# Performance work log

Hardware: AMD Instinct MI355X
Metric: run time of the kernel (lower is better)

Reference implementation:

```python
import jax, jax.numpy as jnp
import numpy as np

N_NODES = 20000
N_EDGES = 160000
N_GRAPHS = 64
EMB_DIM = 16
N_BASIS = 16
MAX_RADIUS = 5.0
MUL_IN = 8   # output_size: multiplicity of scalar atom features
MUL_OUT = 4  # multiplicity per output irrep (4x0e + 4x1o + 4x2e -> dim 36)
W_NUMEL = 3 * MUL_IN * MUL_IN * MUL_OUT  # 768 per-edge tensor-product weights


def setup_inputs() -> dict:
    key = jax.random.key(0)
    ks = jax.random.split(key, 16)
    pos = jax.random.normal(ks[0], (N_NODES, 3), jnp.float32) * 3.0
    A = jax.random.randint(ks[1], (N_NODES,), 0, 10)
    batch = jnp.sort(jax.random.randint(ks[2], (N_NODES,), 0, N_GRAPHS))
    edge_src = jax.random.randint(ks[3], (N_EDGES,), 0, N_NODES)
    edge_dst = jax.random.randint(ks[4], (N_EDGES,), 0, N_NODES)
    edge_shifts = jnp.zeros((N_EDGES, 3), jnp.float32)
    cell = jnp.broadcast_to(jnp.eye(3, dtype=jnp.float32) * 10.0, (N_GRAPHS, 3, 3))
    emb_table = jax.random.normal(ks[5], (10, EMB_DIM), jnp.float32)
    fit_w1 = jax.random.normal(ks[6], (EMB_DIM, 64), jnp.float32) * (2.0 / EMB_DIM) ** 0.5
    fit_b1 = jnp.zeros((64,), jnp.float32)
    fit_w2 = jax.random.normal(ks[7], (64, 32), jnp.float32) * (2.0 / 64.0) ** 0.5
    fit_b2 = jnp.zeros((32,), jnp.float32)
    fit_w3 = jax.random.normal(ks[8], (32, MUL_IN), jnp.float32) * (2.0 / 32.0) ** 0.5
    fit_b3 = jnp.zeros((MUL_IN,), jnp.float32)
    fc_w1 = jax.random.normal(ks[9], (N_BASIS, 64), jnp.float32)
    fc_w2 = jax.random.normal(ks[10], (64, 64), jnp.float32)
    fc_w3 = jax.random.normal(ks[11], (64, 64), jnp.float32)
    fc_w4 = jax.random.normal(ks[12], (64, W_NUMEL), jnp.float32)
    return dict(pos=pos, A=A, batch=batch, edge_src=edge_src, edge_dst=edge_dst,
                edge_shifts=edge_shifts, cell=cell, emb_table=emb_table,
                fit_w1=fit_w1, fit_b1=fit_b1, fit_w2=fit_w2, fit_b2=fit_b2,
                fit_w3=fit_w3, fit_b3=fit_b3,
                fc_w1=fc_w1, fc_w2=fc_w2, fc_w3=fc_w3, fc_w4=fc_w4)


def _forward(pos, edge_shifts, cell, emb_table, fit_w1, fit_b1, fit_w2, fit_b2,
             fit_w3, fit_b3, fc_w1, fc_w2, fc_w3, fc_w4, A, batch, edge_src, edge_dst):
    E = edge_src.shape[0]
    # edge vectors with periodic shifts
    shift = jnp.einsum('ni,nij->nj', edge_shifts, cell[batch[edge_src]])
    ev = pos[edge_dst] - pos[edge_src] + shift                     # [E,3]
    r = jnp.sqrt(jnp.sum(ev * ev, axis=1))                         # [E]
    v = ev / jnp.maximum(r, 1e-9)[:, None]
    x, y, z = v[:, 0], v[:, 1], v[:, 2]
    # spherical harmonics lmax=2, normalize=True, 'component' normalization (e3nn order)
    sh0 = jnp.ones_like(x)                                         # [E]
    sh1 = jnp.sqrt(3.0) * jnp.stack([y, z, x], axis=-1)            # [E,3]
    s15 = jnp.sqrt(15.0); s5 = jnp.sqrt(5.0)
    sh2 = jnp.stack([s15 * x * y, s15 * y * z, (s5 / 2.0) * (3.0 * z * z - 1.0),
                     s15 * x * z, (s15 / 2.0) * (x * x - y * y)], axis=-1)  # [E,5]
    # node scalar features: embedding + fitnet MLP (SiLU)
    h = jax.nn.silu(emb_table[A] @ fit_w1 + fit_b1)
    h = jax.nn.silu(h @ fit_w2 + fit_b2)
    Ai = h @ fit_w3 + fit_b3                                       # [N, MUL_IN]
    # soft_one_hot_linspace(gaussian, cutoff=True) * sqrt(n_basis)
    centers = jnp.linspace(0.0, MAX_RADIUS, N_BASIS + 2)[1:-1]
    step = centers[1] - centers[0]
    rb = jnp.exp(-(((r[:, None] - centers) / step) ** 2)) / 1.12 * jnp.sqrt(jnp.float32(N_BASIS))
    # radial net -> per-edge tensor-product weights (e3nn FullyConnectedNet style, no bias)
    g = jax.nn.silu(rb @ fc_w1 / jnp.sqrt(jnp.float32(N_BASIS)))
    g = jax.nn.silu(g @ fc_w2 / 8.0)
    g = jax.nn.silu(g @ fc_w3 / 8.0)
    w = (g @ fc_w4 / 8.0).reshape(E, 3, MUL_IN, MUL_IN, MUL_OUT)   # [E,3 paths,u,v,w]
    # FullTensorProduct(Ai_src, sh) then FullyConnectedTensorProduct(., Ai_dst) with
    # per-edge weights; scalar x irrep paths factorize: out_l[e,w,m] = S_l[e,w]*sh_l[e,m]
    P = Ai[edge_src][:, :, None] * Ai[edge_dst][:, None, :]        # [E,u,v]
    S = jnp.einsum('euv,eluvw->elw', P, w) / jnp.float32(MUL_IN)   # path norm 1/sqrt(u*v)
    out0 = S[:, 0, :] * sh0[:, None]                               # [E,4]
    out1 = (S[:, 1, :, None] * sh1[:, None, :]).reshape(E, MUL_OUT * 3)
    out2 = (S[:, 2, :, None] * sh2[:, None, :]).reshape(E, MUL_OUT * 5)
    ef = jnp.concatenate([out0, out1, out2], axis=-1)              # [E,36]
    # scatter-mean to destination nodes
    cnt = jnp.clip(jax.ops.segment_sum(jnp.ones((E,), ef.dtype), edge_dst,
                                       num_segments=N_NODES), 1.0)
    return jax.ops.segment_sum(ef, edge_dst, num_segments=N_NODES) / cnt[:, None]


def reference(pos, A, batch, edge_src, edge_dst, edge_shifts, cell, emb_table,
              fit_w1, fit_b1, fit_w2, fit_b2, fit_w3, fit_b3,
              fc_w1, fc_w2, fc_w3, fc_w4):
    return _forward(pos, edge_shifts, cell, emb_table, fit_w1, fit_b1, fit_w2,
                    fit_b2, fit_w3, fit_b3, fc_w1, fc_w2, fc_w3, fc_w4,
                    A, batch, edge_src, edge_dst)
```

## Files before the change

kernel.cpp:

```cpp
#include <hip/hip_runtime.h>
#include <math.h>

#define N_NODES 20000
#define N_EDGES 160000

#define NBINS   512
#define BINS1   513
#define RMAX    7.5f

static const size_t OFF_EF  = 0;
static const size_t OFF_T   = OFF_EF  + (size_t)N_EDGES * 16 * 4;
static const size_t OFF_G   = OFF_T   + (size_t)100 * 64 * 12 * 4;
static const size_t OFF_SV  = OFF_G   + (size_t)64 * BINS1 * 4;
static const size_t OFF_NOFF= OFF_SV  + (size_t)100 * BINS1 * 12 * 4;
static const size_t OFF_NCNT= OFF_NOFF+ (size_t)(N_NODES + 1) * 4;
static const size_t OFF_NCUR= OFF_NCNT+ (size_t)N_NODES * 4;

#define P1_T_BLOCKS  25
#define P1_G_BLOCKS  9
#define P1_H_BLOCKS  625
#define P1_GRID (P1_T_BLOCKS + P1_G_BLOCKS + P1_H_BLOCKS)
#define P2_CHUNKS 9
#define P2_GRID (1 + 100 * P2_CHUNKS)

__device__ __forceinline__ float silu_f(float x) {
    return x / (1.0f + __expf(-x));
}

__global__ __launch_bounds__(256) void prep1_kernel(
        const float* __restrict__ emb,
        const float* __restrict__ fw1, const float* __restrict__ fb1,
        const float* __restrict__ fw2, const float* __restrict__ fb2,
        const float* __restrict__ fw3, const float* __restrict__ fb3,
        const float* __restrict__ fc_w1, const float* __restrict__ fc_w2,
        const float* __restrict__ fc_w3, const float* __restrict__ fc_w4,
        const int* __restrict__ edst,
        float* __restrict__ T, float* __restrict__ g_tT,
        int* __restrict__ cnt_i) {
    __shared__ float smem[4096];
    int b = blockIdx.x;
    int tid = threadIdx.x;

    if (b < P1_T_BLOCKS) {
        float* h1s = smem;
        float* h2s = smem + 640;
        float* ai  = smem + 960;
        for (int idx = tid; idx < 640; idx += 256) {
            int t = idx >> 6, j = idx & 63;
            float acc = fb1[j];
            #pragma unroll
            for (int i = 0; i < 16; i++) acc += emb[t * 16 + i] * fw1[i * 64 + j];
            h1s[idx] = silu_f(acc);
        }
        __syncthreads();
        for (int idx = tid; idx < 320; idx += 256) {
            int t = idx >> 5, j = idx & 31;
            float acc = fb2[j];
            #pragma unroll
            for (int i = 0; i < 64; i++) acc += h1s[t * 64 + i] * fw2[i * 32 + j];
            h2s[idx] = silu_f(acc);
        }
        __syncthreads();
        if (tid < 80) {
            int t = tid >> 3, j = tid & 7;
            float acc = fb3[j];
            #pragma unroll
            for (int i = 0; i < 32; i++) acc += h2s[t * 32 + i] * fw3[i * 8 + j];
            ai[tid] = acc;
        }
        __syncthreads();

        int idx = b * 256 + tid;
        int pair = idx >> 6;
        int k = idx & 63;
        int ts = pair / 10, td = pair - ts * 10;
        float a[8], bb[8];
        #pragma unroll
        for (int i = 0; i < 8; i++) a[i] = ai[ts * 8 + i];
        #pragma unroll
        for (int i = 0; i < 8; i++) bb[i] = ai[td * 8 + i];
        float sv[12];
        #pragma unroll
        for (int i = 0; i < 12; i++) sv[i] = 0.0f;
        const float* wk = fc_w4 + k * 768;
        #pragma unroll 2
        for (int u = 0; u < 8; u++) {
            #pragma unroll
            for (int v = 0; v < 8; v++) {
                float ab = a[u] * bb[v];
                const float* wp = wk + u * 32 + v * 4;
                float4 w0 = *(const float4*)(wp);
                float4 w1 = *(const float4*)(wp + 256);
                float4 w2 = *(const float4*)(wp + 512);
                sv[0] += ab * w0.x; sv[1] += ab * w0.y; sv[2]  += ab * w0.z; sv[3]  += ab * w0.w;
                sv[4] += ab * w1.x; sv[5] += ab * w1.y; sv[6]  += ab * w1.z; sv[7]  += ab * w1.w;
                sv[8] += ab * w2.x; sv[9] += ab * w2.y; sv[10] += ab * w2.z; sv[11] += ab * w2.w;
            }
        }
        float* tp = T + pair * 768 + k * 12;
        #pragma unroll
        for (int j = 0; j < 12; j++) tp[j] = sv[j];
    } else if (b < P1_T_BLOCKS + P1_G_BLOCKS) {
        int lane = tid & 63;
        int wq = __builtin_amdgcn_readfirstlane(tid >> 6);
        int bin = (b - P1_T_BLOCKS) * 64 + lane;
        bool valid = (bin <= NBINS);
        float r = (float)bin * (RMAX / (float)NBINS);

        float rb[16];
        const float step = 5.0f / 17.0f;
        const float istep = 17.0f / 5.0f;
        const float rsc = 4.0f / 1.12f;
        #pragma unroll
        for (int i = 0; i < 16; i++) {
            float dd = (r - (float)(i + 1) * step) * istep;
            rb[i] = __expf(-dd * dd) * rsc;
        }

        #pragma unroll
        for (int jj = 0; jj < 16; jj++) {
            int j = wq * 16 + jj;
            float a0 = 0, a1 = 0, a2 = 0, a3 = 0;
            #pragma unroll
            for (int i = 0; i < 16; i += 4) {
                a0 += rb[i]     * fc_w1[(i)     * 64 + j];
                a1 += rb[i + 1] * fc_w1[(i + 1) * 64 + j];
                a2 += rb[i + 2] * fc_w1[(i + 2) * 64 + j];
                a3 += rb[i + 3] * fc_w1[(i + 3) * 64 + j];
            }
            smem[j * 64 + lane] = silu_f(((a0 + a1) + (a2 + a3)) * 0.25f);
        }
        __syncthreads();

        float acc[16];
        #pragma unroll
        for (int jj = 0; jj < 16; jj++) acc[jj] = 0.0f;
        #pragma unroll
        for (int c = 0; c < 4; c++) {
            float hc[16];
            #pragma unroll
            for (int i = 0; i < 16; i++) hc[i] = smem[(c * 16 + i) * 64 + lane];
            #pragma unroll
            for (int jj = 0; jj < 16; jj++) {
                int j = wq * 16 + jj;
                #pragma unroll
                for (int i = 0; i < 16; i++) acc[jj] += hc[i] * fc_w2[(c * 16 + i) * 64 + j];
            }
        }
        __syncthreads();
        #pragma unroll
        for (int jj = 0; jj < 16; jj++) smem[(wq * 16 + jj) * 64 + lane] = silu_f(acc[jj] * 0.125f);
        __syncthreads();

        #pragma unroll
        for (int jj = 0; jj < 16; jj++) acc[jj] = 0.0f;
        #pragma unroll
        for (int c = 0; c < 4; c++) {
            float hc[16];
            #pragma unroll
            for (int i = 0; i < 16; i++) hc[i] = smem[(c * 16 + i) * 64 + lane];
            #pragma unroll
            for (int jj = 0; jj < 16; jj++) {
                int j = wq * 16 + jj;
                #pragma unroll
                for (int i = 0; i < 16; i++) acc[jj] += hc[i] * fc_w3[(c * 16 + i) * 64 + j];
            }
        }
        if (valid) {
            #pragma unroll
            for (int jj = 0; jj < 16; jj++)
                g_tT[(size_t)(wq * 16 + jj) * BINS1 + bin] = silu_f(acc[jj] * 0.125f);
        }
    } else {
        int e = (b - P1_T_BLOCKS - P1_G_BLOCKS) * 256 + tid;
        if (e < N_EDGES) atomicAdd(&cnt_i[edst[e]], 1);
    }
}

__global__ __launch_bounds__(256) void prep2_kernel(
        const int* __restrict__ cnt_i, int* __restrict__ node_off,
        const float* __restrict__ T, const float* __restrict__ g_tT,
        float* __restrict__ sv_table) {
    __shared__ float smem[4096];
    int b = blockIdx.x;
    int tid = threadIdx.x;

    if (b == 0) {
        int* part = (int*)smem;
        int base = tid * 79;
        int s = 0;
        for (int i = 0; i < 79; i++) {
            int n = base + i;
            if (n < N_NODES) s += cnt_i[n];
        }
        part[tid] = s;
        __syncthreads();
        for (int off = 1; off < 256; off <<= 1) {
            int v = part[tid];
            int add = (tid >= off) ? part[tid - off] : 0;
            __syncthreads();
            part[tid] = v + add;
            __syncthreads();
        }
        int run = (tid == 0) ? 0 : part[tid - 1];
        for (int i = 0; i < 79; i++) {
            int n = base + i;
            if (n < N_NODES) { node_off[n] = run; run += cnt_i[n]; }
        }
        if (tid == 255) node_off[N_NODES] = part[255];
        return;
    }

    int idx = b - 1;
    int pair = idx / P2_CHUNKS;
    int chunk = idx - pair * P2_CHUNKS;

    float* part = smem;
    float* Tlds = smem + 3328;

    const float* Tp = T + pair * 768;
    #pragma unroll
    for (int i = tid; i < 768; i += 256) Tlds[i] = Tp[i];
    __syncthreads();

    int lane = tid & 63;
    int wq = tid >> 6;
    int bin = chunk * 64 + lane;
    bool valid = (bin <= NBINS);
    int rb = valid ? bin : NBINS;

    float acc[12];
    #pragma unroll
    for (int j = 0; j < 12; j++) acc[j] = 0.0f;
    #pragma unroll
    for (int kk = 0; kk < 16; kk++) {
        int k = wq * 16 + kk;
        float g = g_tT[(size_t)k * BINS1 + rb];
        const float* Tl = Tlds + k * 12;
        #pragma unroll
        for (int j = 0; j < 12; j++) acc[j] += g * Tl[j];
    }

    float* pp = part + (size_t)wq * 64 * 13 + (size_t)lane * 13;
    #pragma unroll
    for (int j = 0; j < 12; j++) pp[j] = acc[j];
    __syncthreads();

    const float isc = 1.0f / 64.0f;
    float* svp = sv_table + (size_t)pair * BINS1 * 12 + (size_t)chunk * 64 * 12;
    #pragma unroll
    for (int i = 0; i < 3; i++) {
        int o = tid + 256 * i;
        int bl = o / 12;
        int j = o - bl * 12;
        if (chunk * 64 + bl <= NBINS) {
            float s = part[(size_t)0 * 832 + bl * 13 + j]
                    + part[(size_t)1 * 832 + bl * 13 + j]
                    + part[(size_t)2 * 832 + bl * 13 + j]
                    + part[(size_t)3 * 832 + bl * 13 + j];
            svp[o] = s * isc;
        }
    }
}

__global__ __launch_bounds__(256) void edge_table_kernel(
        const float* __restrict__ pos, const int* __restrict__ batch,
        const int* __restrict__ esrc, const int* __restrict__ edst,
        const float* __restrict__ shifts, const float* __restrict__ cell,
        const int* __restrict__ A,
        const int* __restrict__ node_off, int* __restrict__ node_cur,
        const float* __restrict__ sv_table, float* __restrict__ ef) {
    int e = blockIdx.x * 256 + threadIdx.x;
    if (e >= N_EDGES) return;

    int s = esrc[e], d = edst[e];
    int slot = atomicAdd(&node_cur[d], 1);
    int base = node_off[d];

    int gb = batch[s];
    float t0 = shifts[e * 3 + 0], t1 = shifts[e * 3 + 1], t2 = shifts[e * 3 + 2];
    const float* C = cell + gb * 9;
    float shx = t0 * C[0] + t1 * C[3] + t2 * C[6];
    float shy = t0 * C[1] + t1 * C[4] + t2 * C[7];
    float shz = t0 * C[2] + t1 * C[5] + t2 * C[8];
    float ex = pos[d * 3 + 0] - pos[s * 3 + 0] + shx;
    float ey = pos[d * 3 + 1] - pos[s * 3 + 1] + shy;
    float ez = pos[d * 3 + 2] - pos[s * 3 + 2] + shz;
    float r = sqrtf(ex * ex + ey * ey + ez * ez);
    float inv = 1.0f / fmaxf(r, 1e-9f);
    float x = ex * inv, y = ey * inv, z = ez * inv;

    float sv[12];
    if (r >= RMAX) {
        #pragma unroll
        for (int j = 0; j < 12; j++) sv[j] = 0.0f;
    } else {
        int pair = A[s] * 10 + A[d];
        float t = r * ((float)NBINS / RMAX);
        int i = (int)t;
        i = (i > NBINS - 1) ? (NBINS - 1) : i;
        float f = t - (float)i;
        const float* r0 = sv_table + ((size_t)pair * BINS1 + i) * 12;
        #pragma unroll
        for (int j = 0; j < 12; j++) {
            float lo = r0[j], hi = r0[12 + j];
            sv[j] = lo + f * (hi - lo);
        }
    }

    float4* dst = (float4*)(ef + (size_t)(base + slot) * 16);
    dst[0] = make_float4(sv[0], sv[1], sv[2],  sv[3]);
    dst[1] = make_float4(sv[4], sv[5], sv[6],  sv[7]);
    dst[2] = make_float4(sv[8], sv[9], sv[10], sv[11]);
    dst[3] = make_float4(x, y, z, 0.0f);
}

__global__ __launch_bounds__(256) void gather_kernel(const float* __restrict__ ef,
                                                     const int* __restrict__ node_off,
                                                     float* __restrict__ out) {
    int t = blockIdx.x * 256 + threadIdx.x;
    if (t >= N_NODES * 4) return;
    int n = t >> 2;
    int q = t & 3;
    int beg = node_off[n], end = node_off[n + 1];
    const float4* ef4 = (const float4*)ef;

    const float S3  = 1.7320508075688772f;
    const float S15 = 3.8729833462074170f;
    const float S5  = 2.2360679774997896f;

    float acc[36];
    #pragma unroll
    for (int j = 0; j < 36; j++) acc[j] = 0.0f;

    for (int p = beg + q; p < end; p += 4) {
        const float4* rp = ef4 + (size_t)p * 4;
        float4 svA = rp[0];
        float4 svB = rp[1];
        float4 svC = rp[2];
        float4 dv  = rp[3];
        float x = dv.x, y = dv.y, z = dv.z;
        float sh1v[3] = { S3 * y, S3 * z, S3 * x };
        float sh2v[5] = { S15 * x * y, S15 * y * z, 0.5f * S5 * (3.0f * z * z - 1.0f),
                          S15 * x * z, 0.5f * S15 * (x * x - y * y) };
        acc[0] += svA.x; acc[1] += svA.y; acc[2] += svA.z; acc[3] += svA.w;
        float bw[4] = { svB.x, svB.y, svB.z, svB.w };
        #pragma unroll
        for (int w = 0; w < 4; w++) {
            #pragma unroll
            for (int j = 0; j < 3; j++) acc[4 + w * 3 + j] += bw[w] * sh1v[j];
        }
        float cw[4] = { svC.x, svC.y, svC.z, svC.w };
        #pragma unroll
        for (int w = 0; w < 4; w++) {
            #pragma unroll
            for (int j = 0; j < 5; j++) acc[16 + w * 5 + j] += cw[w] * sh2v[j];
        }
    }

    #pragma unroll
    for (int j = 0; j < 36; j++) {
        acc[j] += __shfl_xor(acc[j], 1);
        acc[j] += __shfl_xor(acc[j], 2);
    }

    if (q == 0) {
        float c = 1.0f / fmaxf((float)(end - beg), 1.0f);
        float4* o4 = (float4*)out + (size_t)n * 9;
        #pragma unroll
        for (int k = 0; k < 9; k++)
            o4[k] = make_float4(acc[k * 4 + 0] * c, acc[k * 4 + 1] * c,
                                acc[k * 4 + 2] * c, acc[k * 4 + 3] * c);
    }
}

extern "C" void kernel_launch(void* const* d_in, const int* in_sizes, int n_in,
                              void* d_out, int out_size, void* d_ws, size_t ws_size,
                              hipStream_t stream) {
    const float* pos    = (const float*)d_in[0];
    const int*   A      = (const int*)d_in[1];
    const int*   batch  = (const int*)d_in[2];
    const int*   esrc   = (const int*)d_in[3];
    const int*   edst   = (const int*)d_in[4];
    const float* shifts = (const float*)d_in[5];
    const float* cell   = (const float*)d_in[6];
    const float* emb    = (const float*)d_in[7];
    const float* fw1    = (const float*)d_in[8];
    const float* fb1    = (const float*)d_in[9];
    const float* fw2    = (const float*)d_in[10];
    const float* fb2    = (const float*)d_in[11];
    const float* fw3    = (const float*)d_in[12];
    const float* fb3    = (const float*)d_in[13];
    const float* fcw1   = (const float*)d_in[14];
    const float* fcw2   = (const float*)d_in[15];
    const float* fcw3   = (const float*)d_in[16];
    const float* fcw4   = (const float*)d_in[17];
    float* out = (float*)d_out;

    char* ws = (char*)d_ws;
    float* ef      = (float*)(ws + OFF_EF);
    float* T       = (float*)(ws + OFF_T);
    float* g_tT    = (float*)(ws + OFF_G);
    float* sv_table= (float*)(ws + OFF_SV);
    int*   node_off= (int*)(ws + OFF_NOFF);
    int*   cnt_i   = (int*)(ws + OFF_NCNT);
    int*   node_cur= (int*)(ws + OFF_NCUR);

    hipMemsetAsync(cnt_i, 0, (size_t)2 * N_NODES * 4, stream);

    prep1_kernel<<<P1_GRID, 256, 0, stream>>>(emb, fw1, fb1, fw2, fb2, fw3, fb3,
                                              fcw1, fcw2, fcw3, fcw4, edst,
                                              T, g_tT, cnt_i);
    prep2_kernel<<<P2_GRID, 256, 0, stream>>>(cnt_i, node_off, T, g_tT, sv_table);
    edge_table_kernel<<<(N_EDGES + 255) / 256, 256, 0, stream>>>(
        pos, batch, esrc, edst, shifts, cell, A, node_off, node_cur, sv_table, ef);
    gather_kernel<<<(N_NODES * 4 + 255) / 256, 256, 0, stream>>>(ef, node_off, out);
}
```

Measured before the change: 191.2 us.

## Parallelize node offset scan across blocks and widen gather to 8 lanes per node

The exclusive scan over per-node edge counts, previously done serially by a single block, is split across 79 blocks. Each block gets its base offset from per-256-node segment counts that prep1 accumulates with extra atomics, and uses wave shuffle scans internally. The gather kernel now assigns 8 threads per destination node instead of 4, adding one shuffle-reduction step. This shortens the single-block critical path in prep2 and raises parallelism in the gather, at the cost of a second atomic per edge and more reduction work.

Result: slower. 292.0 us (+52.7%).

```diff
diff --git a/kernel.cpp b/kernel.cpp
--- a/kernel.cpp
+++ b/kernel.cpp
@@ -15,13 +15,15 @@
 static const size_t OFF_NOFF= OFF_SV  + (size_t)100 * BINS1 * 12 * 4;
 static const size_t OFF_NCNT= OFF_NOFF+ (size_t)(N_NODES + 1) * 4;
 static const size_t OFF_NCUR= OFF_NCNT+ (size_t)N_NODES * 4;
+static const size_t OFF_SEG = OFF_NCUR+ (size_t)N_NODES * 4;
 
 #define P1_T_BLOCKS  25
 #define P1_G_BLOCKS  9
 #define P1_H_BLOCKS  625
 #define P1_GRID (P1_T_BLOCKS + P1_G_BLOCKS + P1_H_BLOCKS)
+#define P2_SCAN_BLOCKS 79
 #define P2_CHUNKS 9
-#define P2_GRID (1 + 100 * P2_CHUNKS)
+#define P2_GRID (P2_SCAN_BLOCKS + 100 * P2_CHUNKS)
 
 __device__ __forceinline__ float silu_f(float x) {
     return x / (1.0f + __expf(-x));
@@ -36,7 +38,7 @@
         const float* __restrict__ fc_w3, const float* __restrict__ fc_w4,
         const int* __restrict__ edst,
         float* __restrict__ T, float* __restrict__ g_tT,
-        int* __restrict__ cnt_i) {
+        int* __restrict__ cnt_i, int* __restrict__ seg_cnt) {
     __shared__ float smem[4096];
     int b = blockIdx.x;
     int tid = threadIdx.x;
@@ -173,45 +175,55 @@
         }
     } else {
         int e = (b - P1_T_BLOCKS - P1_G_BLOCKS) * 256 + tid;
-        if (e < N_EDGES) atomicAdd(&cnt_i[edst[e]], 1);
+        if (e < N_EDGES) {
+            int d = edst[e];
+            atomicAdd(&cnt_i[d], 1);
+            atomicAdd(&seg_cnt[d >> 8], 1);
+        }
     }
 }
 
 __global__ __launch_bounds__(256) void prep2_kernel(
-        const int* __restrict__ cnt_i, int* __restrict__ node_off,
+        const int* __restrict__ cnt_i, const int* __restrict__ seg_cnt,
+        int* __restrict__ node_off,
         const float* __restrict__ T, const float* __restrict__ g_tT,
         float* __restrict__ sv_table) {
     __shared__ float smem[4096];
     int b = blockIdx.x;
     int tid = threadIdx.x;
 
-    if (b == 0) {
-        int* part = (int*)smem;
-        int base = tid * 79;
-        int s = 0;
-        for (int i = 0; i < 79; i++) {
-            int n = base + i;
-            if (n < N_NODES) s += cnt_i[n];
-        }
-        part[tid] = s;
-        __syncthreads();
-        for (int off = 1; off < 256; off <<= 1) {
-            int v = part[tid];
-            int add = (tid >= off) ? part[tid - off] : 0;
-            __syncthreads();
-            part[tid] = v + add;
-            __syncthreads();
-        }
-        int run = (tid == 0) ? 0 : part[tid - 1];
-        for (int i = 0; i < 79; i++) {
-            int n = base + i;
-            if (n < N_NODES) { node_off[n] = run; run += cnt_i[n]; }
-        }
-        if (tid == 255) node_off[N_NODES] = part[255];
+    if (b < P2_SCAN_BLOCKS) {
+        int* ss    = (int*)smem;
+        int* wsum  = (int*)smem + 128;
+        int* basep = (int*)smem + 136;
+        int nbase = b * 256;
+        int n = nbase + tid;
+        if (tid < 80) ss[tid] = (tid < P2_SCAN_BLOCKS) ? seg_cnt[tid] : 0;
+        int c = (n < N_NODES) ? cnt_i[n] : 0;
+        __syncthreads();
+        if (tid == 0) {
+            int s = 0;
+            for (int i = 0; i < b; i++) s += ss[i];
+            basep[0] = s;
+        }
+        int lane = tid & 63, w = tid >> 6;
+        int sc = c;
+        #pragma unroll
+        for (int off = 1; off < 64; off <<= 1) {
+            int v2 = __shfl_up(sc, off);
+            if (lane >= off) sc += v2;
+        }
+        if (lane == 63) wsum[w] = sc;
+        __syncthreads();
+        int wb = 0;
+        #pragma unroll
+        for (int i = 0; i < 4; i++) wb += (i < w) ? wsum[i] : 0;
+        if (n < N_NODES) node_off[n] = basep[0] + wb + (sc - c);
+        if (b == 0 && tid == 0) node_off[N_NODES] = N_EDGES;
         return;
     }
 
-    int idx = b - 1;
+    int idx = b - P2_SCAN_BLOCKS;
     int pair = idx / P2_CHUNKS;
     int chunk = idx - pair * P2_CHUNKS;
 
@@ -319,9 +331,9 @@
                                                      const int* __restrict__ node_off,
                                                      float* __restrict__ out) {
     int t = blockIdx.x * 256 + threadIdx.x;
-    if (t >= N_NODES * 4) return;
-    int n = t >> 2;
-    int q = t & 3;
+    if (t >= N_NODES * 8) return;
+    int n = t >> 3;
+    int q = t & 7;
     int beg = node_off[n], end = node_off[n + 1];
     const float4* ef4 = (const float4*)ef;
 
@@ -333,7 +345,7 @@
     #pragma unroll
     for (int j = 0; j < 36; j++) acc[j] = 0.0f;
 
-    for (int p = beg + q; p < end; p += 4) {
+    for (int p = beg + q; p < end; p += 8) {
         const float4* rp = ef4 + (size_t)p * 4;
         float4 svA = rp[0];
         float4 svB = rp[1];
@@ -362,6 +374,7 @@
     for (int j = 0; j < 36; j++) {
         acc[j] += __shfl_xor(acc[j], 1);
         acc[j] += __shfl_xor(acc[j], 2);
+        acc[j] += __shfl_xor(acc[j], 4);
     }
 
     if (q == 0) {
@@ -405,14 +418,15 @@
     int*   node_off= (int*)(ws + OFF_NOFF);
     int*   cnt_i   = (int*)(ws + OFF_NCNT);
     int*   node_cur= (int*)(ws + OFF_NCUR);
-
-    hipMemsetAsync(cnt_i, 0, (size_t)2 * N_NODES * 4, stream);
+    int*   seg_cnt = (int*)(ws + OFF_SEG);
+
+    hipMemsetAsync(cnt_i, 0, ((size_t)2 * N_NODES + 80) * 4, stream);
 
     prep1_kernel<<<P1_GRID, 256, 0, stream>>>(emb, fw1, fb1, fw2, fb2, fw3, fb3,
                                               fcw1, fcw2, fcw3, fcw4, edst,
-                                              T, g_tT, cnt_i);
-    prep2_kernel<<<P2_GRID, 256, 0, stream>>>(cnt_i, node_off, T, g_tT, sv_table);
+                                              T, g_tT, cnt_i, seg_cnt);
+    prep2_kernel<<<P2_GRID, 256, 0, stream>>>(cnt_i, seg_cnt, node_off, T, g_tT, sv_table);
     edge_table_kernel<<<(N_EDGES + 255) / 256, 256, 0, stream>>>(
         pos, batch, esrc, edst, shifts, cell, A, node_off, node_cur, sv_table, ef);
-    gather_kernel<<<(N_NODES * 4 + 255) / 256, 256, 0, stream>>>(ef, node_off, out);
-}
+    gather_kernel<<<(N_NODES * 8 + 255) / 256, 256, 0, stream>>>(ef, node_off, out);
+}
```
